# Kernel tuning notes

Hardware: AMD Instinct MI355X
Metric: run time of the kernel (lower is better)

## Reference

```python
import jax, jax.numpy as jnp
import numpy as np
from jax import lax

KERNEL = 15
IGNORE = 255


def setup_inputs() -> dict:
    key = jax.random.key(0)
    k1, k2 = jax.random.split(key)
    B, C, H, W = 32, 2, 480, 864
    logits = jax.random.normal(k1, (B, C, H, W), dtype=jnp.float32)
    labels = jax.random.randint(k2, (B, H, W), 0, 2, dtype=jnp.int32)
    return {"logits": logits, "labels": labels}


def _boundary_edgemap(labels):
    # labels: [B, H, W] int32 with values in {0, 1, IGNORE}
    lbl = labels.astype(jnp.int32)
    # np_label = label*255, with ignore pixels set to 0 (matches cv2 path)
    np_label = jnp.where(lbl == IGNORE, 0, lbl * 255)
    win = (1, KERNEL, KERNEL)
    strides = (1, 1, 1)
    # cv2.erode with ones kernel == 15x15 min filter (border value +inf -> pad 255)
    erosion = lax.reduce_window(np_label, jnp.int32(255), lax.min, win, strides, "SAME")
    # cv2.dilate == 15x15 max filter (border value -inf -> pad 0)
    dilation = lax.reduce_window(np_label, jnp.int32(0), lax.max, win, strides, "SAME")
    boundary = dilation - erosion  # >0 exactly on the morphological boundary band
    edgemap = jnp.where(boundary > 0, lbl, IGNORE)
    edgemap = jnp.where(lbl == IGNORE, IGNORE, edgemap)
    return edgemap


def reference(logits, labels):
    # logits: [B, C, H, W] log-probabilities, labels: [B, H, W]
    edgemap = _boundary_edgemap(labels)  # [B, H, W]
    valid = edgemap != IGNORE
    tgt = jnp.where(valid, edgemap, 0)  # safe index for ignored pixels
    # gather logits[b, tgt, h, w] -> [B, H, W]
    picked = jnp.take_along_axis(logits, tgt[:, None, :, :], axis=1)[:, 0]
    # NLLLoss with ignore_index: mean of -logp over valid pixels
    n_valid = jnp.maximum(jnp.sum(valid), 1)
    loss = -jnp.sum(jnp.where(valid, picked, 0.0)) / n_valid.astype(logits.dtype)
    return loss
```

## Files before the change

kernel.cpp:

```cpp
#include <hip/hip_runtime.h>


namespace {
constexpr int B_ = 32;
constexpr int H_ = 480;
constexpr int W_ = 864;
constexpr int TW = 64;
constexpr int TH = 32;
constexpr int R_ = 7;
constexpr int LH = TH + 2 * R_;
constexpr int WC = 20;
constexpr int HC = TW / 4;
constexpr int GX = (W_ + TW - 1) / TW;
constexpr int GY = H_ / TH;
constexpr int NBLK = GX * GY * B_;
}

__device__ __forceinline__ unsigned fold4(unsigned x) {
  x |= x >> 16;
  x |= x >> 8;
  return x & 0xFFu;
}

__device__ __forceinline__ unsigned flag_of(int v) {
  return (v == 0 || v == 255) ? 1u : (v == 1 ? 2u : 0u);
}

extern "C" __global__ __launch_bounds__(256, 4)
void boundary_loss_main(const float* __restrict__ logits,
                        const int* __restrict__ labels,
                        double2* __restrict__ partials)
{
  __shared__ unsigned sflag[LH][WC];
  __shared__ unsigned sraw[LH][WC];
  __shared__ unsigned hfl[LH][HC];
  __shared__ double red_s[4];
  __shared__ unsigned red_c[4];

  const int tid = threadIdx.x;
  const int tile_w = blockIdx.x * TW;
  const int tile_h = blockIdx.y * TH;
  const int b = blockIdx.z;

  const int* __restrict__ lab = labels + (size_t)b * H_ * W_;

  for (int it = tid; it < LH * WC; it += 256) {
    const int r = it / WC;
    const int wc = it - r * WC;
    const int gh = tile_h - R_ + r;
    const int gw = tile_w - 8 + wc * 4;
    unsigned raw = 0xC8C8C8C8u;
    unsigned flg = 0u;
    if (gh >= 0 && gh < H_ && gw >= 0 && gw < W_) {
      const int4 v = *(const int4*)(lab + (size_t)gh * W_ + gw);
      raw = (unsigned)(v.x & 0xFF) | ((unsigned)(v.y & 0xFF) << 8) |
            ((unsigned)(v.z & 0xFF) << 16) | ((unsigned)(v.w & 0xFF) << 24);
      flg = flag_of(v.x) | (flag_of(v.y) << 8) | (flag_of(v.z) << 16) |
            (flag_of(v.w) << 24);
    }
    sraw[r][wc] = raw;
    sflag[r][wc] = flg;
  }
  __syncthreads();

  for (int it = tid; it < LH * HC; it += 256) {
    const int r = it >> 4;
    const int wc = it & 15;
    const unsigned w0 = sflag[r][wc];
    const unsigned w1 = sflag[r][wc + 1];
    const unsigned w2 = sflag[r][wc + 2];
    const unsigned w3 = sflag[r][wc + 3];
    const unsigned w4 = sflag[r][wc + 4];
    const unsigned core = fold4(w1 | w2 | w3);
    const unsigned o0 = core | fold4(w0 >> 8);
    const unsigned o1 = core | fold4(w0 >> 16) | (w4 & 0xFFu);
    const unsigned o2 = core | (w0 >> 24) | fold4(w4 & 0xFFFFu);
    const unsigned o3 = core | fold4(w4 & 0xFFFFFFu);
    hfl[r][wc] = o0 | (o1 << 8) | (o2 << 16) | (o3 << 24);
  }
  __syncthreads();

  double lsum = 0.0;
  unsigned lcnt = 0;
  const float* __restrict__ lg0 = logits + (size_t)b * 2 * H_ * W_;
  const float* __restrict__ lg1 = lg0 + (size_t)H_ * W_;

  for (int it = tid; it < TH * HC; it += 256) {
    const int r = it >> 4;
    const int wc = it & 15;
    const int gw0 = tile_w + wc * 4;
    if (gw0 < W_) {
      unsigned acc = 0;
#pragma unroll
      for (int k = 0; k < 15; ++k) acc |= hfl[r + k][wc];
      const unsigned craw = sraw[r + R_][wc + 2];
      const int gh = tile_h + r;
      const size_t off = (size_t)gh * W_ + gw0;
      const float4 v0 = *(const float4*)(lg0 + off);
      const float4 v1 = *(const float4*)(lg1 + off);
      const float c0[4] = {v0.x, v0.y, v0.z, v0.w};
      const float c1[4] = {v1.x, v1.y, v1.z, v1.w};
#pragma unroll
      for (int j = 0; j < 4; ++j) {
        const unsigned fb = (acc >> (8 * j)) & 0xFFu;
        const unsigned lv = (craw >> (8 * j)) & 0xFFu;
        if (fb == 3u && lv != 255u) {
          lsum += (double)(lv ? c1[j] : c0[j]);
          ++lcnt;
        }
      }
    }
  }

#pragma unroll
  for (int off = 32; off > 0; off >>= 1) {
    lsum += __shfl_down(lsum, off, 64);
    lcnt += __shfl_down(lcnt, off, 64);
  }
  const int wave = tid >> 6;
  if ((tid & 63) == 0) { red_s[wave] = lsum; red_c[wave] = lcnt; }
  __syncthreads();
  if (tid == 0) {
    const double s = red_s[0] + red_s[1] + red_s[2] + red_s[3];
    const double c = (double)(red_c[0] + red_c[1] + red_c[2] + red_c[3]);
    const int bid = (blockIdx.z * GY + blockIdx.y) * GX + blockIdx.x;
    partials[bid] = make_double2(s, c);
  }
}

extern "C" __global__ __launch_bounds__(1024)
void boundary_loss_final(const double2* __restrict__ partials,
                         float* __restrict__ out)
{
  __shared__ double red_s[16];
  __shared__ double red_c[16];
  const int tid = threadIdx.x;
  double s = 0.0, c = 0.0;
  for (int i = tid; i < NBLK; i += 1024) {
    const double2 p = partials[i];
    s += p.x;
    c += p.y;
  }
#pragma unroll
  for (int off = 32; off > 0; off >>= 1) {
    s += __shfl_down(s, off, 64);
    c += __shfl_down(c, off, 64);
  }
  const int wave = tid >> 6;
  if ((tid & 63) == 0) { red_s[wave] = s; red_c[wave] = c; }
  __syncthreads();
  if (tid == 0) {
    double ts = 0.0, tc = 0.0;
#pragma unroll
    for (int i = 0; i < 16; ++i) { ts += red_s[i]; tc += red_c[i]; }
    if (tc < 1.0) tc = 1.0;
    out[0] = (float)(-ts / tc);
  }
}

extern "C" void kernel_launch(void* const* d_in, const int* in_sizes, int n_in,
                              void* d_out, int out_size, void* d_ws, size_t ws_size,
                              hipStream_t stream)
{
  const float* logits = (const float*)d_in[0];
  const int* labels = (const int*)d_in[1];
  float* out = (float*)d_out;
  double2* partials = (double2*)d_ws;

  dim3 grid(GX, GY, B_);
  boundary_loss_main<<<grid, 256, 0, stream>>>(logits, labels, partials);
  boundary_loss_final<<<1, 1024, 0, stream>>>(partials, out);
}
```

Before: 195.3 us.

## Prefetch logits before label staging and unroll loads for latency overlap

Result: no change. 194.1 us (-0.6%).

```diff
diff --git a/kernel.cpp b/kernel.cpp
--- a/kernel.cpp
+++ b/kernel.cpp
@@ -26,7 +26,7 @@
   return (v == 0 || v == 255) ? 1u : (v == 1 ? 2u : 0u);
 }
 
-extern "C" __global__ __launch_bounds__(256, 4)
+extern "C" __global__ __launch_bounds__(256, 8)
 void boundary_loss_main(const float* __restrict__ logits,
                         const int* __restrict__ labels,
                         double2* __restrict__ partials)
@@ -43,23 +43,50 @@
   const int b = blockIdx.z;
 
   const int* __restrict__ lab = labels + (size_t)b * H_ * W_;
+  const float* __restrict__ lg0 = logits + (size_t)b * 2 * H_ * W_;
+  const float* __restrict__ lg1 = lg0 + (size_t)H_ * W_;
 
-  for (int it = tid; it < LH * WC; it += 256) {
+  int4 lv[4];
+#pragma unroll
+  for (int u = 0; u < 4; ++u) {
+    const int it = tid + 256 * u;
     const int r = it / WC;
-    const int wc = it - r * WC;
+    const int wcc = it - r * WC;
     const int gh = tile_h - R_ + r;
-    const int gw = tile_w - 8 + wc * 4;
-    unsigned raw = 0xC8C8C8C8u;
-    unsigned flg = 0u;
-    if (gh >= 0 && gh < H_ && gw >= 0 && gw < W_) {
-      const int4 v = *(const int4*)(lab + (size_t)gh * W_ + gw);
-      raw = (unsigned)(v.x & 0xFF) | ((unsigned)(v.y & 0xFF) << 8) |
-            ((unsigned)(v.z & 0xFF) << 16) | ((unsigned)(v.w & 0xFF) << 24);
-      flg = flag_of(v.x) | (flag_of(v.y) << 8) | (flag_of(v.z) << 16) |
-            (flag_of(v.w) << 24);
+    const int gw = tile_w - 8 + wcc * 4;
+    lv[u] = make_int4(200, 200, 200, 200);
+    if (it < LH * WC && gh >= 0 && gh < H_ && gw >= 0 && gw < W_)
+      lv[u] = *(const int4*)(lab + (size_t)gh * W_ + gw);
+  }
+
+  const int r0 = tid >> 4;
+  const int wcp = tid & 15;
+  const int gw0 = tile_w + wcp * 4;
+  const bool inb = gw0 < W_;
+  float4 pA0 = make_float4(0, 0, 0, 0), pA1 = pA0, pB0 = pA0, pB1 = pA0;
+  if (inb) {
+    const size_t offA = (size_t)(tile_h + r0) * W_ + gw0;
+    const size_t offB = offA + (size_t)16 * W_;
+    pA0 = *(const float4*)(lg0 + offA);
+    pA1 = *(const float4*)(lg1 + offA);
+    pB0 = *(const float4*)(lg0 + offB);
+    pB1 = *(const float4*)(lg1 + offB);
+  }
+
+#pragma unroll
+  for (int u = 0; u < 4; ++u) {
+    const int it = tid + 256 * u;
+    if (it < LH * WC) {
+      const int r = it / WC;
+      const int wcc = it - r * WC;
+      const int4 v = lv[u];
+      const unsigned raw = (unsigned)(v.x & 0xFF) | ((unsigned)(v.y & 0xFF) << 8) |
+                           ((unsigned)(v.z & 0xFF) << 16) | ((unsigned)(v.w & 0xFF) << 24);
+      const unsigned flg = flag_of(v.x) | (flag_of(v.y) << 8) |
+                           (flag_of(v.z) << 16) | (flag_of(v.w) << 24);
+      sraw[r][wcc] = raw;
+      sflag[r][wcc] = flg;
     }
-    sraw[r][wc] = raw;
-    sflag[r][wc] = flg;
   }
   __syncthreads();
 
@@ -82,33 +109,31 @@
 
   double lsum = 0.0;
   unsigned lcnt = 0;
-  const float* __restrict__ lg0 = logits + (size_t)b * 2 * H_ * W_;
-  const float* __restrict__ lg1 = lg0 + (size_t)H_ * W_;
-
-  for (int it = tid; it < TH * HC; it += 256) {
-    const int r = it >> 4;
-    const int wc = it & 15;
-    const int gw0 = tile_w + wc * 4;
-    if (gw0 < W_) {
-      unsigned acc = 0;
+  if (inb) {
+    unsigned accA = 0, accB = 0;
 #pragma unroll
-      for (int k = 0; k < 15; ++k) acc |= hfl[r + k][wc];
-      const unsigned craw = sraw[r + R_][wc + 2];
-      const int gh = tile_h + r;
-      const size_t off = (size_t)gh * W_ + gw0;
-      const float4 v0 = *(const float4*)(lg0 + off);
-      const float4 v1 = *(const float4*)(lg1 + off);
-      const float c0[4] = {v0.x, v0.y, v0.z, v0.w};
-      const float c1[4] = {v1.x, v1.y, v1.z, v1.w};
+    for (int k = 0; k < 15; ++k) {
+      accA |= hfl[r0 + k][wcp];
+      accB |= hfl[r0 + 16 + k][wcp];
+    }
+    const unsigned crawA = sraw[r0 + R_][wcp + 2];
+    const unsigned crawB = sraw[r0 + 16 + R_][wcp + 2];
+    const float cA0[4] = {pA0.x, pA0.y, pA0.z, pA0.w};
+    const float cA1[4] = {pA1.x, pA1.y, pA1.z, pA1.w};
+    const float cB0[4] = {pB0.x, pB0.y, pB0.z, pB0.w};
+    const float cB1[4] = {pB1.x, pB1.y, pB1.z, pB1.w};
 #pragma unroll
-      for (int j = 0; j < 4; ++j) {
-        const unsigned fb = (acc >> (8 * j)) & 0xFFu;
-        const unsigned lv = (craw >> (8 * j)) & 0xFFu;
-        if (fb == 3u && lv != 255u) {
-          lsum += (double)(lv ? c1[j] : c0[j]);
-          ++lcnt;
-        }
-      }
+    for (int j = 0; j < 4; ++j) {
+      const unsigned fA = (accA >> (8 * j)) & 0xFFu;
+      const unsigned lA = (crawA >> (8 * j)) & 0xFFu;
+      const bool okA = (fA == 3u) && (lA != 255u);
+      lsum += okA ? (double)(lA ? cA1[j] : cA0[j]) : 0.0;
+      lcnt += okA;
+      const unsigned fB = (accB >> (8 * j)) & 0xFFu;
+      const unsigned lB = (crawB >> (8 * j)) & 0xFFu;
+      const bool okB = (fB == 3u) && (lB != 255u);
+      lsum += okB ? (double)(lB ? cB1[j] : cB0[j]) : 0.0;
+      lcnt += okB;
     }
   }
 
```

## Prefetch logits early, transpose flags to column bytes, cut syncs and LDS

Applied to the files above, without the earlier changes.

New measurement: 201.9 us. +3.4%, slower.

```diff
diff --git a/kernel.cpp b/kernel.cpp
--- a/kernel.cpp
+++ b/kernel.cpp
@@ -10,10 +10,11 @@
 constexpr int R_ = 7;
 constexpr int LH = TH + 2 * R_;
 constexpr int WC = 20;
-constexpr int HC = TW / 4;
+constexpr int CPW = 13;
 constexpr int GX = (W_ + TW - 1) / TW;
 constexpr int GY = H_ / TH;
 constexpr int NBLK = GX * GY * B_;
+constexpr int NPART = NBLK * 4;
 }
 
 __device__ __forceinline__ unsigned fold4(unsigned x) {
@@ -22,92 +23,125 @@
   return x & 0xFFu;
 }
 
-__device__ __forceinline__ unsigned flag_of(int v) {
-  return (v == 0 || v == 255) ? 1u : (v == 1 ? 2u : 0u);
-}
-
-extern "C" __global__ __launch_bounds__(256, 4)
+__device__ __forceinline__ unsigned flag3(int v) {
+  return (v == 0) ? 1u : ((v == 1) ? 2u : ((v == 255) ? 5u : 0u));
+}
+
+extern "C" __global__ __launch_bounds__(256, 6)
 void boundary_loss_main(const float* __restrict__ logits,
                         const int* __restrict__ labels,
                         double2* __restrict__ partials)
 {
   __shared__ unsigned sflag[LH][WC];
-  __shared__ unsigned sraw[LH][WC];
-  __shared__ unsigned hfl[LH][HC];
-  __shared__ double red_s[4];
-  __shared__ unsigned red_c[4];
+  __shared__ unsigned colbuf[TW][CPW];
 
   const int tid = threadIdx.x;
+  const int wv = tid >> 6;
+  const int lane = tid & 63;
   const int tile_w = blockIdx.x * TW;
   const int tile_h = blockIdx.y * TH;
   const int b = blockIdx.z;
 
   const int* __restrict__ lab = labels + (size_t)b * H_ * W_;
-
-  for (int it = tid; it < LH * WC; it += 256) {
-    const int r = it / WC;
-    const int wc = it - r * WC;
-    const int gh = tile_h - R_ + r;
-    const int gw = tile_w - 8 + wc * 4;
-    unsigned raw = 0xC8C8C8C8u;
-    unsigned flg = 0u;
-    if (gh >= 0 && gh < H_ && gw >= 0 && gw < W_) {
-      const int4 v = *(const int4*)(lab + (size_t)gh * W_ + gw);
-      raw = (unsigned)(v.x & 0xFF) | ((unsigned)(v.y & 0xFF) << 8) |
-            ((unsigned)(v.z & 0xFF) << 16) | ((unsigned)(v.w & 0xFF) << 24);
-      flg = flag_of(v.x) | (flag_of(v.y) << 8) | (flag_of(v.z) << 16) |
-            (flag_of(v.w) << 24);
-    }
-    sraw[r][wc] = raw;
-    sflag[r][wc] = flg;
-  }
-  __syncthreads();
-
-  for (int it = tid; it < LH * HC; it += 256) {
-    const int r = it >> 4;
-    const int wc = it & 15;
-    const unsigned w0 = sflag[r][wc];
-    const unsigned w1 = sflag[r][wc + 1];
-    const unsigned w2 = sflag[r][wc + 2];
-    const unsigned w3 = sflag[r][wc + 3];
-    const unsigned w4 = sflag[r][wc + 4];
-    const unsigned core = fold4(w1 | w2 | w3);
-    const unsigned o0 = core | fold4(w0 >> 8);
-    const unsigned o1 = core | fold4(w0 >> 16) | (w4 & 0xFFu);
-    const unsigned o2 = core | (w0 >> 24) | fold4(w4 & 0xFFFFu);
-    const unsigned o3 = core | fold4(w4 & 0xFFFFFFu);
-    hfl[r][wc] = o0 | (o1 << 8) | (o2 << 16) | (o3 << 24);
+  const float* __restrict__ lg0 = logits + (size_t)b * 2 * H_ * W_;
+  const float* __restrict__ lg1 = lg0 + (size_t)H_ * W_;
+
+  const int c = tid & 63;
+  const int q = tid >> 6;
+  const int gw = tile_w + c;
+  const bool inb = gw < W_;
+  float L0[8], L1[8];
+  if (inb) {
+    const float* p0 = lg0 + (size_t)(tile_h + 8 * q) * W_ + gw;
+    const float* p1 = lg1 + (size_t)(tile_h + 8 * q) * W_ + gw;
+#pragma unroll
+    for (int rr = 0; rr < 8; ++rr) { L0[rr] = p0[(size_t)rr * W_]; L1[rr] = p1[(size_t)rr * W_]; }
+  } else {
+#pragma unroll
+    for (int rr = 0; rr < 8; ++rr) { L0[rr] = 0.f; L1[rr] = 0.f; }
+  }
+
+  const int row0 = wv * 12;
+  const int nrows = (LH - row0) < 12 ? (LH - row0) : 12;
+  int4 lv[4];
+#pragma unroll
+  for (int u = 0; u < 4; ++u) {
+    const int idx = u * 64 + lane;
+    lv[u] = make_int4(200, 200, 200, 200);
+    if (idx < nrows * WC) {
+      const int r = row0 + idx / WC;
+      const int wc = idx % WC;
+      const int gh = tile_h - R_ + r;
+      const int gwl = tile_w - 8 + wc * 4;
+      if (gh >= 0 && gh < H_ && gwl >= 0 && gwl < W_)
+        lv[u] = *(const int4*)(lab + (size_t)gh * W_ + gwl);
+    }
+  }
+#pragma unroll
+  for (int u = 0; u < 4; ++u) {
+    const int idx = u * 64 + lane;
+    if (idx < nrows * WC) {
+      const int r = row0 + idx / WC;
+      const int wc = idx % WC;
+      const int4 v = lv[u];
+      sflag[r][wc] = flag3(v.x) | (flag3(v.y) << 8) | (flag3(v.z) << 16) |
+                     (flag3(v.w) << 24);
+    }
+  }
+
+  unsigned char* cb = (unsigned char*)&colbuf[0][0];
+#pragma unroll
+  for (int u = 0; u < 3; ++u) {
+    const int idx = u * 64 + lane;
+    if (idx < nrows * 16) {
+      const int r = row0 + (idx >> 4);
+      const int wc = idx & 15;
+      const unsigned w0 = sflag[r][wc];
+      const unsigned w1 = sflag[r][wc + 1];
+      const unsigned w2 = sflag[r][wc + 2];
+      const unsigned w3 = sflag[r][wc + 3];
+      const unsigned w4 = sflag[r][wc + 4];
+      const unsigned core = fold4(w1 | w2 | w3);
+      const unsigned o0 = core | fold4(w0 >> 8);
+      const unsigned o1 = core | fold4(w0 >> 16) | (w4 & 0xFFu);
+      const unsigned o2 = core | (w0 >> 24) | fold4(w4 & 0xFFFFu);
+      const unsigned o3 = core | fold4(w4 & 0xFFFFFFu);
+      const int cbase = 4 * wc;
+      cb[(cbase + 0) * 52 + r] = (unsigned char)((o0 & 3u) | ((w2 & 7u) << 2));
+      cb[(cbase + 1) * 52 + r] = (unsigned char)((o1 & 3u) | (((w2 >> 8) & 7u) << 2));
+      cb[(cbase + 2) * 52 + r] = (unsigned char)((o2 & 3u) | (((w2 >> 16) & 7u) << 2));
+      cb[(cbase + 3) * 52 + r] = (unsigned char)((o3 & 3u) | (((w2 >> 24) & 7u) << 2));
+    }
   }
   __syncthreads();
 
   double lsum = 0.0;
   unsigned lcnt = 0;
-  const float* __restrict__ lg0 = logits + (size_t)b * 2 * H_ * W_;
-  const float* __restrict__ lg1 = lg0 + (size_t)H_ * W_;
-
-  for (int it = tid; it < TH * HC; it += 256) {
-    const int r = it >> 4;
-    const int wc = it & 15;
-    const int gw0 = tile_w + wc * 4;
-    if (gw0 < W_) {
-      unsigned acc = 0;
-#pragma unroll
-      for (int k = 0; k < 15; ++k) acc |= hfl[r + k][wc];
-      const unsigned craw = sraw[r + R_][wc + 2];
-      const int gh = tile_h + r;
-      const size_t off = (size_t)gh * W_ + gw0;
-      const float4 v0 = *(const float4*)(lg0 + off);
-      const float4 v1 = *(const float4*)(lg1 + off);
-      const float c0[4] = {v0.x, v0.y, v0.z, v0.w};
-      const float c1[4] = {v1.x, v1.y, v1.z, v1.w};
+  if (inb) {
+    unsigned d[6];
+#pragma unroll
+    for (int k = 0; k < 6; ++k) d[k] = colbuf[c][2 * q + k];
+#pragma unroll
+    for (int m = 0; m < 2; ++m) {
+      const unsigned M = 0x03030303u;
+      const unsigned A0 = d[m] & M, A1 = d[m + 1] & M, A2 = d[m + 2] & M,
+                     A3 = d[m + 3] & M, A4 = d[m + 4] & M;
+      const unsigned Cc = fold4(A1 | A2);
+      const unsigned f3v = fold4(A3);
+      const unsigned o0 = fold4(A0) | Cc | fold4(A3 & 0x00FFFFFFu);
+      const unsigned o1 = fold4(A0 >> 8) | Cc | f3v;
+      const unsigned o2 = fold4(A0 >> 16) | Cc | f3v | (A4 & 0xFFu);
+      const unsigned o3 = (A0 >> 24) | Cc | f3v | fold4(A4 & 0xFFFFu);
+      const unsigned cen = (d[m + 1] >> 24) | (d[m + 2] << 8);
+      const unsigned ov[4] = {o0, o1, o2, o3};
 #pragma unroll
       for (int j = 0; j < 4; ++j) {
-        const unsigned fb = (acc >> (8 * j)) & 0xFFu;
-        const unsigned lv = (craw >> (8 * j)) & 0xFFu;
-        if (fb == 3u && lv != 255u) {
-          lsum += (double)(lv ? c1[j] : c0[j]);
-          ++lcnt;
-        }
+        const unsigned cbj = (cen >> (8 * j)) & 0xFFu;
+        const bool valid = (ov[j] == 3u) && ((cbj & 0x10u) == 0u);
+        const int rr = 4 * m + j;
+        const float v = (cbj & 0x08u) ? L1[rr] : L0[rr];
+        lsum += valid ? (double)v : 0.0;
+        lcnt += valid;
       }
     }
   }
@@ -117,14 +151,9 @@
     lsum += __shfl_down(lsum, off, 64);
     lcnt += __shfl_down(lcnt, off, 64);
   }
-  const int wave = tid >> 6;
-  if ((tid & 63) == 0) { red_s[wave] = lsum; red_c[wave] = lcnt; }
-  __syncthreads();
-  if (tid == 0) {
-    const double s = red_s[0] + red_s[1] + red_s[2] + red_s[3];
-    const double c = (double)(red_c[0] + red_c[1] + red_c[2] + red_c[3]);
+  if (lane == 0) {
     const int bid = (blockIdx.z * GY + blockIdx.y) * GX + blockIdx.x;
-    partials[bid] = make_double2(s, c);
+    partials[bid * 4 + wv] = make_double2(lsum, (double)lcnt);
   }
 }
 
@@ -135,19 +164,19 @@
   __shared__ double red_s[16];
   __shared__ double red_c[16];
   const int tid = threadIdx.x;
-  double s = 0.0, c = 0.0;
-  for (int i = tid; i < NBLK; i += 1024) {
+  double s = 0.0, cc = 0.0;
+  for (int i = tid; i < NPART; i += 1024) {
     const double2 p = partials[i];
     s += p.x;
-    c += p.y;
+    cc += p.y;
   }
 #pragma unroll
   for (int off = 32; off > 0; off >>= 1) {
     s += __shfl_down(s, off, 64);
-    c += __shfl_down(c, off, 64);
+    cc += __shfl_down(cc, off, 64);
   }
   const int wave = tid >> 6;
-  if ((tid & 63) == 0) { red_s[wave] = s; red_c[wave] = c; }
+  if ((tid & 63) == 0) { red_s[wave] = s; red_c[wave] = cc; }
   __syncthreads();
   if (tid == 0) {
     double ts = 0.0, tc = 0.0;
```
